# Kernel tuning notes

Measured on AMD Instinct MI355X. Metric: run time of the kernel, lower is better.

## Reference

```python
import jax, jax.numpy as jnp
import numpy as np
from jax import lax

GAMMA = 1.0

def _conv(x, w, b, stride, pad):
    y = lax.conv_general_dilated(x, w, (stride, stride), [(pad, pad), (pad, pad)],
                                 dimension_numbers=('NCHW', 'OIHW', 'NCHW'))
    return y + b[None, :, None, None]

def _maxpool2s1(x):
    return lax.reduce_window(x, -jnp.inf, lax.max, (1, 1, 2, 2), (1, 1, 1, 1), 'VALID')

def setup_inputs() -> dict:
    key = jax.random.key(0)
    ks = jax.random.split(key, 13)
    d = {}
    d['x'] = jax.random.normal(ks[0], (128, 3, 250, 250), dtype=jnp.float32)
    d['conv1_w'] = jax.random.normal(ks[1], (6, 3, 5, 5), dtype=jnp.float32) / np.sqrt(3 * 25)
    d['conv1_b'] = jax.random.normal(ks[2], (6,), dtype=jnp.float32) * 0.01
    d['conv2_w'] = jax.random.normal(ks[3], (15, 6, 3, 3), dtype=jnp.float32) / np.sqrt(6 * 9)
    d['conv2_b'] = jax.random.normal(ks[4], (15,), dtype=jnp.float32) * 0.01
    d['fc1_w'] = jax.random.normal(ks[5], (120, 55815), dtype=jnp.float32) / np.sqrt(55815.0)
    d['fc1_b'] = jax.random.normal(ks[6], (120,), dtype=jnp.float32) * 0.01
    d['fc2_w'] = jax.random.normal(ks[7], (84, 120), dtype=jnp.float32) / np.sqrt(120.0)
    d['fc2_b'] = jax.random.normal(ks[8], (84,), dtype=jnp.float32) * 0.01
    d['fc3_w'] = jax.random.normal(ks[9], (1, 84), dtype=jnp.float32) / np.sqrt(84.0)
    d['fc3_b'] = jax.random.normal(ks[10], (1,), dtype=jnp.float32) * 0.01
    d['support'] = jax.random.normal(ks[11], (10, 1), dtype=jnp.float32)
    return d

def reference(x, conv1_w, conv1_b, conv2_w, conv2_b, fc1_w, fc1_b, fc2_w, fc2_b, fc3_w, fc3_b, support):
    h = jax.nn.relu(_conv(x, conv1_w, conv1_b, 2, 1))   # [B,6,124,124]
    h = _maxpool2s1(h)                                   # [B,6,123,123] (dropout = identity in eval)
    h = jax.nn.relu(_conv(h, conv2_w, conv2_b, 2, 1))    # [B,15,62,62]
    h = _maxpool2s1(h)                                   # [B,15,61,61]
    h = h.reshape(h.shape[0], -1)                        # [B,55815]
    h = jax.nn.relu(h @ fc1_w.T + fc1_b)
    h = jax.nn.relu(h @ fc2_w.T + fc2_b)
    h = h @ fc3_w.T + fc3_b                              # [B,1]
    # fused RBF kernel vs support set: k[i,j] = exp(-gamma*(x_i - s_j)^2)
    diff = h - support[:, 0][None, :]                    # [B,10]
    k = jnp.exp(-GAMMA * diff * diff)
    h = k.mean(axis=1, keepdims=True)                    # [B,1]
    probs = jax.nn.sigmoid(h)
    return jnp.concatenate((probs, 1.0 - probs), axis=-1)  # [B,2]
```

## Files before the change

### kernel.cpp

```cpp
#include <hip/hip_runtime.h>
#include <math.h>


#define BATCH 128

#define C1_ST 82
#define C1_COLS 69
#define C1_ROWS 67
#define C1_TOT (C1_ROWS * C1_COLS)
__global__ __launch_bounds__(128) void conv1_pool_kernel(
    const float* __restrict__ x, const float* __restrict__ w,
    const float* __restrict__ bias, float* __restrict__ out) {
  const int b = blockIdx.z;
  const int P0 = blockIdx.x * 32;
  const int R0 = blockIdx.y * 31;
  const int tid = threadIdx.x;
  const int t = tid >> 3;
  const int s = tid & 7;

  __shared__ float lds[C1_ROWS * C1_ST];
  float* cbuf = lds;

  float acc0[5][6], acc1[5][6];
#pragma unroll
  for (int oc = 0; oc < 6; oc++) {
    float bv = bias[oc];
#pragma unroll
    for (int dc = 0; dc < 5; dc++) { acc0[dc][oc] = bv; acc1[dc][oc] = bv; }
  }

  const int ihb = 2 * R0 - 1, iwb = 2 * P0 - 1;

#pragma unroll 1
  for (int ci = 0; ci < 3; ci++) {
    __syncthreads();
    const float* src = x + (size_t)(b * 3 + ci) * 62500;
#pragma unroll 1
    for (int base = tid; base < C1_TOT; base += 1024) {
      float vv[8];
      int lrv[8], ilv[8];
#pragma unroll
      for (int k = 0; k < 8; k++) {
        int i = base + (k << 7);
        int lr = (int)(((unsigned)i * 121575u) >> 23);
        int il = i - lr * 69;
        lrv[k] = lr; ilv[k] = il;
        int ih = ihb + lr, iw = iwb + il;
        bool ok = (i < C1_TOT) && ((unsigned)ih < 250u) && ((unsigned)iw < 250u);
        vv[k] = ok ? src[ih * 250 + iw] : 0.f;
      }
#pragma unroll
      for (int k = 0; k < 8; k++) {
        int i = base + (k << 7);
        if (i < C1_TOT) lds[lrv[k] * C1_ST + ilv[k] + (ilv[k] >> 3)] = vv[k];
      }
    }
    __syncthreads();

#pragma unroll 1
    for (int ir = 0; ir < 7; ir++) {
      const float* rp = &lds[(4 * t + ir) * C1_ST + 9 * s];
      float v[13];
#pragma unroll
      for (int j = 0; j < 13; j++) v[j] = rp[j + (j >> 3)];

      if (ir < 5) {
#pragma unroll
        for (int oc = 0; oc < 6; oc++) {
          const float* wr = w + ((oc * 3 + ci) * 5 + ir) * 5;
          float w0 = wr[0], w1 = wr[1], w2 = wr[2], w3 = wr[3], w4 = wr[4];
#pragma unroll
          for (int dc = 0; dc < 5; dc++) {
            float a = acc0[dc][oc];
            a += w0 * v[2 * dc + 0];
            a += w1 * v[2 * dc + 1];
            a += w2 * v[2 * dc + 2];
            a += w3 * v[2 * dc + 3];
            a += w4 * v[2 * dc + 4];
            acc0[dc][oc] = a;
          }
        }
      }
      if (ir >= 2) {
#pragma unroll
        for (int oc = 0; oc < 6; oc++) {
          const float* wr = w + ((oc * 3 + ci) * 5 + (ir - 2)) * 5;
          float w0 = wr[0], w1 = wr[1], w2 = wr[2], w3 = wr[3], w4 = wr[4];
#pragma unroll
          for (int dc = 0; dc < 5; dc++) {
            float a = acc1[dc][oc];
            a += w0 * v[2 * dc + 0];
            a += w1 * v[2 * dc + 1];
            a += w2 * v[2 * dc + 2];
            a += w3 * v[2 * dc + 3];
            a += w4 * v[2 * dc + 4];
            acc1[dc][oc] = a;
          }
        }
      }
    }
  }

  __syncthreads();
#pragma unroll
  for (int oc = 0; oc < 6; oc++)
#pragma unroll
    for (int dc = 0; dc < 5; dc++)
      cbuf[tid * 31 + oc * 5 + dc] = acc0[dc][oc];

  const int p0 = R0 + 2 * t;
  const int c0 = P0 + 4 * s;
  if (p0 < 123) {
#pragma unroll
    for (int oc = 0; oc < 6; oc++) {
      float* orow = out + ((size_t)(b * 6 + oc) * 123 + p0) * 123;
      float m0 = fmaxf(fmaxf(fmaxf(acc0[0][oc], acc0[1][oc]),
                             fmaxf(acc1[0][oc], acc1[1][oc])), 0.f);
      float m1 = fmaxf(fmaxf(fmaxf(acc0[1][oc], acc0[2][oc]),
                             fmaxf(acc1[1][oc], acc1[2][oc])), 0.f);
      float m2 = fmaxf(fmaxf(fmaxf(acc0[2][oc], acc0[3][oc]),
                             fmaxf(acc1[2][oc], acc1[3][oc])), 0.f);
      float m3 = fmaxf(fmaxf(fmaxf(acc0[3][oc], acc0[4][oc]),
                             fmaxf(acc1[3][oc], acc1[4][oc])), 0.f);
      if (c0 + 3 < 123) {
        *(float4*)&orow[c0] = make_float4(m0, m1, m2, m3);
      } else {
        if (c0 < 123) orow[c0] = m0;
        if (c0 + 1 < 123) orow[c0 + 1] = m1;
        if (c0 + 2 < 123) orow[c0 + 2] = m2;
      }
    }
  }

  __syncthreads();
  if (t < 15 && p0 + 1 < 123) {
    const float* nb = &cbuf[(tid + 8) * 31];
#pragma unroll
    for (int oc = 0; oc < 6; oc++) {
      float n0 = nb[oc * 5 + 0], n1 = nb[oc * 5 + 1], n2 = nb[oc * 5 + 2];
      float n3 = nb[oc * 5 + 3], n4 = nb[oc * 5 + 4];
      float* orow = out + ((size_t)(b * 6 + oc) * 123 + p0 + 1) * 123;
      float m0 = fmaxf(fmaxf(fmaxf(acc1[0][oc], acc1[1][oc]), fmaxf(n0, n1)), 0.f);
      float m1 = fmaxf(fmaxf(fmaxf(acc1[1][oc], acc1[2][oc]), fmaxf(n1, n2)), 0.f);
      float m2 = fmaxf(fmaxf(fmaxf(acc1[2][oc], acc1[3][oc]), fmaxf(n2, n3)), 0.f);
      float m3 = fmaxf(fmaxf(fmaxf(acc1[3][oc], acc1[4][oc]), fmaxf(n3, n4)), 0.f);
      if (c0 + 3 < 123) {
        *(float4*)&orow[c0] = make_float4(m0, m1, m2, m3);
      } else {
        if (c0 < 123) orow[c0] = m0;
        if (c0 + 1 < 123) orow[c0 + 1] = m1;
        if (c0 + 2 < 123) orow[c0 + 2] = m2;
      }
    }
  }
}

#define C2_ST 84
#define C2_TOT (35 * 67)
__global__ __launch_bounds__(256) void conv2_pool_kernel(
    const float* __restrict__ in, const float* __restrict__ w,
    const float* __restrict__ bias, float* __restrict__ out) {
  const int b = blockIdx.z;
  const int P0 = blockIdx.x * 32;
  const int R0 = blockIdx.y * 16;
  const int tid = threadIdx.x;
  const int t = tid >> 4;
  const int s = tid & 15;

  __shared__ float lds[35 * C2_ST];

  const int ihb = 2 * R0 - 1, iwb = 2 * P0 - 1;
  const int r = R0 + t;
  const int c0 = P0 + 2 * s;

#pragma unroll 1
  for (int ocg = 0; ocg < 2; ocg++) {
    const int oc0 = ocg * 7;
    float acc0[3][8], acc1[3][8];
#pragma unroll
    for (int k = 0; k < 8; k++) {
      float bv = bias[oc0 + k];
#pragma unroll
      for (int dc = 0; dc < 3; dc++) { acc0[dc][k] = bv; acc1[dc][k] = bv; }
    }

#pragma unroll 1
    for (int ci = 0; ci < 6; ci++) {
      __syncthreads();
      const float* src = in + (size_t)(b * 6 + ci) * 15129;
#pragma unroll 1
      for (int base = tid; base < C2_TOT; base += 2048) {
        float vv[8];
        int lrv[8], ilv[8];
#pragma unroll
        for (int k = 0; k < 8; k++) {
          int i = base + (k << 8);
          int lr = (int)(((unsigned)i * 125204u) >> 23);
          int il = i - lr * 67;
          lrv[k] = lr; ilv[k] = il;
          int ih = ihb + lr, iw = iwb + il;
          bool ok = (i < C2_TOT) && ((unsigned)ih < 123u) && ((unsigned)iw < 123u);
          vv[k] = ok ? src[ih * 123 + iw] : 0.f;
        }
#pragma unroll
        for (int k = 0; k < 8; k++) {
          int i = base + (k << 8);
          if (i < C2_TOT) lds[lrv[k] * C2_ST + ilv[k] + (ilv[k] >> 2)] = vv[k];
        }
      }
      __syncthreads();

#pragma unroll 1
      for (int ir = 0; ir < 5; ir++) {
        const float* rp = &lds[(2 * t + ir) * C2_ST + 5 * s];
        float v[7];
#pragma unroll
        for (int j = 0; j < 7; j++) v[j] = rp[j + (j >> 2)];

        if (ir < 3) {
#pragma unroll
          for (int k = 0; k < 8; k++) {
            const float* wr = w + (((oc0 + k) * 6 + ci) * 3 + ir) * 3;
            float w0 = wr[0], w1 = wr[1], w2 = wr[2];
#pragma unroll
            for (int dc = 0; dc < 3; dc++) {
              float a = acc0[dc][k];
              a += w0 * v[2 * dc + 0];
              a += w1 * v[2 * dc + 1];
              a += w2 * v[2 * dc + 2];
              acc0[dc][k] = a;
            }
          }
        }
        if (ir >= 2) {
#pragma unroll
          for (int k = 0; k < 8; k++) {
            const float* wr = w + (((oc0 + k) * 6 + ci) * 3 + (ir - 2)) * 3;
            float w0 = wr[0], w1 = wr[1], w2 = wr[2];
#pragma unroll
            for (int dc = 0; dc < 3; dc++) {
              float a = acc1[dc][k];
              a += w0 * v[2 * dc + 0];
              a += w1 * v[2 * dc + 1];
              a += w2 * v[2 * dc + 2];
              acc1[dc][k] = a;
            }
          }
        }
      }
    }

    if (r < 61) {
#pragma unroll
      for (int k = 0; k < 8; k++) {
        int oc = oc0 + k;
        float* orow = out + ((size_t)(b * 15 + oc) * 61 + r) * 61;
        float m0 = fmaxf(fmaxf(fmaxf(acc0[0][k], acc0[1][k]),
                               fmaxf(acc1[0][k], acc1[1][k])), 0.f);
        float m1 = fmaxf(fmaxf(fmaxf(acc0[1][k], acc0[2][k]),
                               fmaxf(acc1[1][k], acc1[2][k])), 0.f);
        if (c0 + 1 < 61) {
          *(float2*)&orow[c0] = make_float2(m0, m1);
        } else if (c0 < 61) {
          orow[c0] = m0;
        }
      }
    }
  }
}

#define KTOT 55815
#define NPART 512
#define KCHUNK 112
__global__ __launch_bounds__(512) void fc1_splitk_kernel(
    const float* __restrict__ act, const float* __restrict__ w,
    float* __restrict__ partial) {
  const int kbase = blockIdx.x * KCHUNK;
  const int tid = threadIdx.x;
  const int tx = tid & 31, ty = tid >> 5;
  __shared__ float ldsA[8 * 132];
  __shared__ float ldsB[8 * 132];
  float acc[8][4];
#pragma unroll
  for (int i = 0; i < 8; i++)
#pragma unroll
    for (int j = 0; j < 4; j++) acc[i][j] = 0.f;

  for (int s8 = 0; s8 < KCHUNK / 8; s8++) {
    int kofs = kbase + s8 * 8;
    __syncthreads();
    for (int i = tid; i < 1024; i += 512) {
      int m = i >> 3, kk = i & 7;
      int k = kofs + kk;
      ldsA[kk * 132 + m] = (k < KTOT) ? act[m * KTOT + k] : 0.f;
    }
    for (int i = tid; i < 960; i += 512) {
      int n = i >> 3, kk = i & 7;
      int k = kofs + kk;
      ldsB[kk * 132 + n] = (k < KTOT) ? w[n * KTOT + k] : 0.f;
    }
    __syncthreads();
#pragma unroll
    for (int kk = 0; kk < 8; kk++) {
      float4 a0 = *(const float4*)&ldsA[kk * 132 + ty * 8];
      float4 a1 = *(const float4*)&ldsA[kk * 132 + ty * 8 + 4];
      float4 b0 = *(const float4*)&ldsB[kk * 132 + tx * 4];
      float av[8] = {a0.x, a0.y, a0.z, a0.w, a1.x, a1.y, a1.z, a1.w};
      float bv[4] = {b0.x, b0.y, b0.z, b0.w};
#pragma unroll
      for (int i = 0; i < 8; i++)
#pragma unroll
        for (int j = 0; j < 4; j++) acc[i][j] += av[i] * bv[j];
    }
  }

  if (tx < 30) {
    float* dst = partial + (size_t)blockIdx.x * 15360;
#pragma unroll
    for (int i = 0; i < 8; i++) {
      int row = ty * 8 + i;
      float4 st = make_float4(acc[i][0], acc[i][1], acc[i][2], acc[i][3]);
      *(float4*)&dst[row * 120 + tx * 4] = st;
    }
  }
}

__global__ __launch_bounds__(64) void fc1_reduce1_kernel(
    const float* __restrict__ partial, float* __restrict__ partial2) {
  int idx = blockIdx.x * 64 + threadIdx.x;
  int g = blockIdx.y;
  const float* p = partial + (size_t)g * 64 * 15360 + idx;
  float s = 0.f;
#pragma unroll 8
  for (int q = 0; q < 64; q++) s += p[(size_t)q * 15360];
  partial2[(size_t)g * 15360 + idx] = s;
}

__global__ __launch_bounds__(64) void fc1_reduce2_kernel(
    const float* __restrict__ partial2, const float* __restrict__ bias,
    float* __restrict__ h1) {
  int idx = blockIdx.x * 64 + threadIdx.x;
  float s = 0.f;
#pragma unroll
  for (int g = 0; g < 8; g++) s += partial2[(size_t)g * 15360 + idx];
  h1[idx] = fmaxf(s + bias[idx % 120], 0.f);
}

__global__ __launch_bounds__(128) void head_kernel(
    const float* __restrict__ h1, const float* __restrict__ fc2_w,
    const float* __restrict__ fc2_b, const float* __restrict__ fc3_w,
    const float* __restrict__ fc3_b, const float* __restrict__ support,
    float* __restrict__ out) {
  int b = blockIdx.x, t = threadIdx.x;
  __shared__ float hrow[120];
  __shared__ float s2[84];
  if (t < 120) hrow[t] = h1[b * 120 + t];
  __syncthreads();
  if (t < 84) {
    float d = fc2_b[t];
    for (int k = 0; k < 120; k++) d += fc2_w[t * 120 + k] * hrow[k];
    s2[t] = fmaxf(d, 0.f);
  }
  __syncthreads();
  if (t == 0) {
    float h = fc3_b[0];
    for (int j = 0; j < 84; j++) h += fc3_w[j] * s2[j];
    float ks = 0.f;
    for (int j = 0; j < 10; j++) {
      float diff = h - support[j];
      ks += expf(-diff * diff);
    }
    ks *= 0.1f;
    float p = 1.f / (1.f + expf(-ks));
    out[b * 2] = p;
    out[b * 2 + 1] = 1.f - p;
  }
}

extern "C" void kernel_launch(void* const* d_in, const int* in_sizes, int n_in,
                              void* d_out, int out_size, void* d_ws, size_t ws_size,
                              hipStream_t stream) {
  const float* x   = (const float*)d_in[0];
  const float* c1w = (const float*)d_in[1];
  const float* c1b = (const float*)d_in[2];
  const float* c2w = (const float*)d_in[3];
  const float* c2b = (const float*)d_in[4];
  const float* f1w = (const float*)d_in[5];
  const float* f1b = (const float*)d_in[6];
  const float* f2w = (const float*)d_in[7];
  const float* f2b = (const float*)d_in[8];
  const float* f3w = (const float*)d_in[9];
  const float* f3b = (const float*)d_in[10];
  const float* sup = (const float*)d_in[11];
  float* out = (float*)d_out;

  char* ws = (char*)d_ws;
  float* pool1 = (float*)ws;
  float* act   = (float*)(ws + 46476288);
  float* part  = (float*)ws;
  float* h1    = (float*)(ws + 33000000);
  float* part2 = (float*)(ws + 34000000);

  conv1_pool_kernel<<<dim3(4, 4, BATCH), 128, 0, stream>>>(x, c1w, c1b, pool1);
  conv2_pool_kernel<<<dim3(2, 4, BATCH), 256, 0, stream>>>(pool1, c2w, c2b, act);
  fc1_splitk_kernel<<<NPART, 512, 0, stream>>>(act, f1w, part);
  fc1_reduce1_kernel<<<dim3(240, 8), 64, 0, stream>>>(part, part2);
  fc1_reduce2_kernel<<<240, 64, 0, stream>>>(part2, f1b, h1);
  head_kernel<<<BATCH, 128, 0, stream>>>(h1, f2w, f2b, f3w, f3b, sup, out);
}
```

Baseline: 359.3 us.

## Give each conv1 thread one conv row and exchange pool neighbours via shuffles

The conv1+pool kernel moves from 128 to 256 threads per block. Each thread now computes a single conv output row segment instead of two, which halves the accumulator registers and drops the 7-row loop with its conditional branches. The vertical max-pool neighbour row comes from __shfl_down within the wavefront, and LDS is used only at wave boundaries. The LDS stride and padding also change to a 16-column skew. The intent is higher occupancy and less redundant work per thread, at the cost of more threads each doing less and some added shuffle/LDS edge handling.

```diff
diff --git a/kernel.cpp b/kernel.cpp
--- a/kernel.cpp
+++ b/kernel.cpp
@@ -4,11 +4,11 @@
 
 #define BATCH 128
 
-#define C1_ST 82
+#define C1_ST 74
 #define C1_COLS 69
 #define C1_ROWS 67
 #define C1_TOT (C1_ROWS * C1_COLS)
-__global__ __launch_bounds__(128) void conv1_pool_kernel(
+__global__ __launch_bounds__(256, 8) void conv1_pool_kernel(
     const float* __restrict__ x, const float* __restrict__ w,
     const float* __restrict__ bias, float* __restrict__ out) {
   const int b = blockIdx.z;
@@ -21,12 +21,12 @@
   __shared__ float lds[C1_ROWS * C1_ST];
   float* cbuf = lds;
 
-  float acc0[5][6], acc1[5][6];
+  float acc[5][6];
 #pragma unroll
   for (int oc = 0; oc < 6; oc++) {
     float bv = bias[oc];
 #pragma unroll
-    for (int dc = 0; dc < 5; dc++) { acc0[dc][oc] = bv; acc1[dc][oc] = bv; }
+    for (int dc = 0; dc < 5; dc++) acc[dc][oc] = bv;
   }
 
   const int ihb = 2 * R0 - 1, iwb = 2 * P0 - 1;
@@ -36,12 +36,12 @@
     __syncthreads();
     const float* src = x + (size_t)(b * 3 + ci) * 62500;
 #pragma unroll 1
-    for (int base = tid; base < C1_TOT; base += 1024) {
+    for (int base = tid; base < C1_TOT; base += 2048) {
       float vv[8];
       int lrv[8], ilv[8];
 #pragma unroll
       for (int k = 0; k < 8; k++) {
-        int i = base + (k << 7);
+        int i = base + (k << 8);
         int lr = (int)(((unsigned)i * 121575u) >> 23);
         int il = i - lr * 69;
         lrv[k] = lr; ilv[k] = il;
@@ -51,99 +51,74 @@
       }
 #pragma unroll
       for (int k = 0; k < 8; k++) {
-        int i = base + (k << 7);
-        if (i < C1_TOT) lds[lrv[k] * C1_ST + ilv[k] + (ilv[k] >> 3)] = vv[k];
+        int i = base + (k << 8);
+        if (i < C1_TOT) lds[lrv[k] * C1_ST + ilv[k] + (ilv[k] >> 4)] = vv[k];
       }
     }
     __syncthreads();
 
-#pragma unroll 1
-    for (int ir = 0; ir < 7; ir++) {
-      const float* rp = &lds[(4 * t + ir) * C1_ST + 9 * s];
+    const float* rbase = &lds[(2 * t) * C1_ST + 8 * s + (s >> 1)];
+    const int hfix = s & 1;
+#pragma unroll
+    for (int ir = 0; ir < 5; ir++) {
+      const float* rpl = rbase + ir * C1_ST;
+      const float* rph = rpl + hfix;
       float v[13];
 #pragma unroll
-      for (int j = 0; j < 13; j++) v[j] = rp[j + (j >> 3)];
-
-      if (ir < 5) {
-#pragma unroll
-        for (int oc = 0; oc < 6; oc++) {
-          const float* wr = w + ((oc * 3 + ci) * 5 + ir) * 5;
-          float w0 = wr[0], w1 = wr[1], w2 = wr[2], w3 = wr[3], w4 = wr[4];
-#pragma unroll
-          for (int dc = 0; dc < 5; dc++) {
-            float a = acc0[dc][oc];
-            a += w0 * v[2 * dc + 0];
-            a += w1 * v[2 * dc + 1];
-            a += w2 * v[2 * dc + 2];
-            a += w3 * v[2 * dc + 3];
-            a += w4 * v[2 * dc + 4];
-            acc0[dc][oc] = a;
-          }
-        }
-      }
-      if (ir >= 2) {
-#pragma unroll
-        for (int oc = 0; oc < 6; oc++) {
-          const float* wr = w + ((oc * 3 + ci) * 5 + (ir - 2)) * 5;
-          float w0 = wr[0], w1 = wr[1], w2 = wr[2], w3 = wr[3], w4 = wr[4];
-#pragma unroll
-          for (int dc = 0; dc < 5; dc++) {
-            float a = acc1[dc][oc];
-            a += w0 * v[2 * dc + 0];
-            a += w1 * v[2 * dc + 1];
-            a += w2 * v[2 * dc + 2];
-            a += w3 * v[2 * dc + 3];
-            a += w4 * v[2 * dc + 4];
-            acc1[dc][oc] = a;
-          }
+      for (int j = 0; j < 8; j++)  v[j] = rpl[j];
+#pragma unroll
+      for (int j = 8; j < 13; j++) v[j] = rph[j];
+#pragma unroll
+      for (int oc = 0; oc < 6; oc++) {
+        const float* wr = w + ((oc * 3 + ci) * 5 + ir) * 5;
+        float w0 = wr[0], w1 = wr[1], w2 = wr[2], w3 = wr[3], w4 = wr[4];
+#pragma unroll
+        for (int dc = 0; dc < 5; dc++) {
+          float a = acc[dc][oc];
+          a += w0 * v[2 * dc + 0];
+          a += w1 * v[2 * dc + 1];
+          a += w2 * v[2 * dc + 2];
+          a += w3 * v[2 * dc + 3];
+          a += w4 * v[2 * dc + 4];
+          acc[dc][oc] = a;
         }
       }
     }
   }
 
   __syncthreads();
-#pragma unroll
-  for (int oc = 0; oc < 6; oc++)
-#pragma unroll
-    for (int dc = 0; dc < 5; dc++)
-      cbuf[tid * 31 + oc * 5 + dc] = acc0[dc][oc];
-
-  const int p0 = R0 + 2 * t;
+  if (t == 8 || t == 16 || t == 24) {
+    float* cb = &cbuf[(((t >> 3) - 1) * 8 + s) * 30];
+#pragma unroll
+    for (int oc = 0; oc < 6; oc++)
+#pragma unroll
+      for (int dc = 0; dc < 5; dc++) cb[oc * 5 + dc] = acc[dc][oc];
+  }
+  __syncthreads();
+
+  const int p0 = R0 + t;
   const int c0 = P0 + 4 * s;
-  if (p0 < 123) {
-#pragma unroll
-    for (int oc = 0; oc < 6; oc++) {
+  const bool edge = ((t & 7) == 7) && (t < 31);
+  const bool wr_ok = (t < 31) && (p0 < 123);
+  const float* cb = &cbuf[((t >> 3) * 8 + s) * 30];
+
+#pragma unroll
+  for (int oc = 0; oc < 6; oc++) {
+    float a0 = acc[0][oc], a1 = acc[1][oc], a2 = acc[2][oc],
+          a3 = acc[3][oc], a4 = acc[4][oc];
+    float n0 = __shfl_down(a0, 8), n1 = __shfl_down(a1, 8),
+          n2 = __shfl_down(a2, 8), n3 = __shfl_down(a3, 8),
+          n4 = __shfl_down(a4, 8);
+    if (edge) {
+      n0 = cb[oc * 5 + 0]; n1 = cb[oc * 5 + 1]; n2 = cb[oc * 5 + 2];
+      n3 = cb[oc * 5 + 3]; n4 = cb[oc * 5 + 4];
+    }
+    if (wr_ok) {
       float* orow = out + ((size_t)(b * 6 + oc) * 123 + p0) * 123;
-      float m0 = fmaxf(fmaxf(fmaxf(acc0[0][oc], acc0[1][oc]),
-                             fmaxf(acc1[0][oc], acc1[1][oc])), 0.f);
-      float m1 = fmaxf(fmaxf(fmaxf(acc0[1][oc], acc0[2][oc]),
-                             fmaxf(acc1[1][oc], acc1[2][oc])), 0.f);
-      float m2 = fmaxf(fmaxf(fmaxf(acc0[2][oc], acc0[3][oc]),
-                             fmaxf(acc1[2][oc], acc1[3][oc])), 0.f);
-      float m3 = fmaxf(fmaxf(fmaxf(acc0[3][oc], acc0[4][oc]),
-                             fmaxf(acc1[3][oc], acc1[4][oc])), 0.f);
-      if (c0 + 3 < 123) {
-        *(float4*)&orow[c0] = make_float4(m0, m1, m2, m3);
-      } else {
-        if (c0 < 123) orow[c0] = m0;
-        if (c0 + 1 < 123) orow[c0 + 1] = m1;
-        if (c0 + 2 < 123) orow[c0 + 2] = m2;
-      }
-    }
-  }
-
-  __syncthreads();
-  if (t < 15 && p0 + 1 < 123) {
-    const float* nb = &cbuf[(tid + 8) * 31];
-#pragma unroll
-    for (int oc = 0; oc < 6; oc++) {
-      float n0 = nb[oc * 5 + 0], n1 = nb[oc * 5 + 1], n2 = nb[oc * 5 + 2];
-      float n3 = nb[oc * 5 + 3], n4 = nb[oc * 5 + 4];
-      float* orow = out + ((size_t)(b * 6 + oc) * 123 + p0 + 1) * 123;
-      float m0 = fmaxf(fmaxf(fmaxf(acc1[0][oc], acc1[1][oc]), fmaxf(n0, n1)), 0.f);
-      float m1 = fmaxf(fmaxf(fmaxf(acc1[1][oc], acc1[2][oc]), fmaxf(n1, n2)), 0.f);
-      float m2 = fmaxf(fmaxf(fmaxf(acc1[2][oc], acc1[3][oc]), fmaxf(n2, n3)), 0.f);
-      float m3 = fmaxf(fmaxf(fmaxf(acc1[3][oc], acc1[4][oc]), fmaxf(n3, n4)), 0.f);
+      float m0 = fmaxf(fmaxf(fmaxf(a0, a1), fmaxf(n0, n1)), 0.f);
+      float m1 = fmaxf(fmaxf(fmaxf(a1, a2), fmaxf(n1, n2)), 0.f);
+      float m2 = fmaxf(fmaxf(fmaxf(a2, a3), fmaxf(n2, n3)), 0.f);
+      float m3 = fmaxf(fmaxf(fmaxf(a3, a4), fmaxf(n3, n4)), 0.f);
       if (c0 + 3 < 123) {
         *(float4*)&orow[c0] = make_float4(m0, m1, m2, m3);
       } else {
@@ -401,7 +376,7 @@
   float* h1    = (float*)(ws + 33000000);
   float* part2 = (float*)(ws + 34000000);
 
-  conv1_pool_kernel<<<dim3(4, 4, BATCH), 128, 0, stream>>>(x, c1w, c1b, pool1);
+  conv1_pool_kernel<<<dim3(4, 4, BATCH), 256, 0, stream>>>(x, c1w, c1b, pool1);
   conv2_pool_kernel<<<dim3(2, 4, BATCH), 256, 0, stream>>>(pool1, c2w, c2b, act);
   fc1_splitk_kernel<<<NPART, 512, 0, stream>>>(act, f1w, part);
   fc1_reduce1_kernel<<<dim3(240, 8), 64, 0, stream>>>(part, part2);
```

Result: slower. 521.9 us (+45.2%).
